# Performance work log

Hardware: AMD Instinct MI355X
Metric: run time of the kernel (lower is better)

## Reference

```python
import jax, jax.numpy as jnp
import numpy as np
import math

BT, N, D, H = 16, 1024, 128, 8
HD = D // H


def setup_inputs() -> dict:
    key = jax.random.key(0)
    ks = jax.random.split(key, 12)
    s = 1.0 / math.sqrt(D)
    return {
        "x": jax.random.normal(ks[0], (BT, N, D), dtype=jnp.float32),
        "adj": jax.random.uniform(ks[1], (BT, N, N), dtype=jnp.float32),
        "Wq": jax.random.normal(ks[2], (D, D), dtype=jnp.float32) * s,
        "bq": jax.random.normal(ks[3], (D,), dtype=jnp.float32) * 0.01,
        "Wk": jax.random.normal(ks[4], (D, D), dtype=jnp.float32) * s,
        "bk": jax.random.normal(ks[5], (D,), dtype=jnp.float32) * 0.01,
        "Wv": jax.random.normal(ks[6], (D, D), dtype=jnp.float32) * s,
        "bv": jax.random.normal(ks[7], (D,), dtype=jnp.float32) * 0.01,
        "Wo": jax.random.normal(ks[8], (D, D), dtype=jnp.float32) * s,
        "bo": jax.random.normal(ks[9], (D,), dtype=jnp.float32) * 0.01,
    }


def reference(x, adj, Wq, bq, Wk, bk, Wv, bv, Wo, bo):
    bt, n, d = x.shape
    # projections (torch Linear: x @ W.T + b), split into heads -> (BT,H,N,HD)
    q = (x @ Wq.T + bq).reshape(bt, n, H, HD).transpose(0, 2, 1, 3)
    k = (x @ Wk.T + bk).reshape(bt, n, H, HD).transpose(0, 2, 1, 3)
    v = (x @ Wv.T + bv).reshape(bt, n, H, HD).transpose(0, 2, 1, 3)
    scores = jnp.einsum('bhnd,bhmd->bhnm', q, k) / math.sqrt(HD)  # (BT,H,N,N)
    mask = (adj == 0)[:, None, :, :]  # (BT,1,N,N)
    scores = jnp.where(mask, -jnp.inf, scores)
    attn = jax.nn.softmax(scores, axis=-1)
    attn = attn * adj[:, None, :, :]  # reweight by continuous causal strength
    attn = attn / (attn.sum(axis=-1, keepdims=True) + 1e-8)  # renormalize
    ctx = jnp.einsum('bhnm,bhmd->bhnd', attn, v)  # (BT,H,N,HD)
    ctx = ctx.transpose(0, 2, 1, 3).reshape(bt, n, d)
    return ctx @ Wo.T + bo
```

## Files before the change

kernel.cpp:

```cpp
#include <hip/hip_runtime.h>
#include <hip/hip_bf16.h>

#define BTC 16
#define NC 1024
#define DC 128
#define HC 8
#define HDC 16

typedef __attribute__((ext_vector_type(8)))  short bf16x8;
typedef __attribute__((ext_vector_type(4)))  float f32x4;
typedef __attribute__((ext_vector_type(16))) float f32x16;
typedef __attribute__((ext_vector_type(4)))  short short4v;

#if __has_builtin(__builtin_amdgcn_exp2f)
#define EXP2F(x) __builtin_amdgcn_exp2f(x)
#else
#define EXP2F(x) exp2f(x)
#endif

#define QSCALE 0.36067376022224085f

union PK2 { short4v s4; __hip_bfloat162 h2[2]; };
union PK8 { bf16x8 v; short s[8]; __hip_bfloat162 h2[4]; };

static __device__ inline short f2bf(float f) {
    unsigned u = __builtin_bit_cast(unsigned, f);
    u += 0x7fffu + ((u >> 16) & 1u);
    return (short)(u >> 16);
}

static __device__ inline bf16x8 pack8f(float4 a, float4 b) {
    PK8 f;
    f.h2[0] = __float22bfloat162_rn(make_float2(a.x, a.y));
    f.h2[1] = __float22bfloat162_rn(make_float2(a.z, a.w));
    f.h2[2] = __float22bfloat162_rn(make_float2(b.x, b.y));
    f.h2[3] = __float22bfloat162_rn(make_float2(b.z, b.w));
    return f.v;
}

__global__ __launch_bounds__(256)
void proj_qkv(const float* __restrict__ x,
              const float* __restrict__ Wq, const float* __restrict__ bq,
              const float* __restrict__ Wk, const float* __restrict__ bk,
              const float* __restrict__ Wv, const float* __restrict__ bv,
              short* __restrict__ qo, short* __restrict__ ko, short* __restrict__ vto)
{
    const int y = blockIdx.y;
    const float* W    = (y == 0) ? Wq : (y == 1) ? Wk : Wv;
    const float* bias = (y == 0) ? bq : (y == 1) ? bk : bv;
    const float scale = (y == 0) ? QSCALE : 1.0f;

    const int tid  = threadIdx.x;
    const int wave = tid >> 6;
    const int lane = tid & 63;
    const int l15  = lane & 15;
    const int quad = lane >> 4;
    const int rowA = blockIdx.x * 64 + wave * 16;

    f32x4 acc[8];
#pragma unroll
    for (int t = 0; t < 8; ++t) acc[t] = (f32x4){0.f, 0.f, 0.f, 0.f};

#pragma unroll
    for (int kk = 0; kk < DC; kk += 32) {
        const float* xp = &x[(size_t)(rowA + l15) * DC + kk + quad * 8];
        bf16x8 Af = pack8f(*(const float4*)xp, *(const float4*)(xp + 4));
#pragma unroll
        for (int t = 0; t < 8; ++t) {
            const float* wp = &W[(size_t)(t * 16 + l15) * DC + kk + quad * 8];
            bf16x8 Bf = pack8f(*(const float4*)wp, *(const float4*)(wp + 4));
            acc[t] = __builtin_amdgcn_mfma_f32_16x16x32_bf16(Af, Bf, acc[t], 0, 0, 0);
        }
    }

#pragma unroll
    for (int t = 0; t < 8; ++t) {
        int c = t * 16 + l15;
        float b = bias[c];
#pragma unroll
        for (int r = 0; r < 4; ++r) {
            int row = rowA + quad * 4 + r;
            float val = (acc[t][r] + b) * scale;
            if (y == 2)
                vto[(size_t)(row >> 10) * (DC * NC) + (size_t)c * NC + (row & (NC - 1))] = f2bf(val);
            else
                ((y == 0) ? qo : ko)[(size_t)row * DC + c] = f2bf(val);
        }
    }
}

__global__ __launch_bounds__(512, 4)
void attn_fused(const short* __restrict__ qb, const short* __restrict__ kb,
                const short* __restrict__ vt, const float* __restrict__ adj,
                const float* __restrict__ Wo, const float* __restrict__ bo,
                float* __restrict__ out)
{
    __shared__ float As[2][32 * 132];
    __shared__ short Ps[8][32 * 40];
    __shared__ short Cs[32 * 136];

    const int tid  = threadIdx.x;
    const int wave = tid >> 6;
    const int lane = tid & 63;
    const int l15  = lane & 15;
    const int quad = lane >> 4;
    const int l31  = lane & 31;
    const int lh   = lane >> 5;
    const int bt   = blockIdx.y;
    const int qt0  = blockIdx.x * 32;
    const int h    = wave;

    const size_t xb = (size_t)bt * NC * DC;
    const size_t ab = (size_t)bt * NC * NC;

    bf16x8 Bq = *(const bf16x8*)&qb[xb + (size_t)(qt0 + l31) * DC + h * HDC + lh * 8];

    PK8 ones;
#pragma unroll
    for (int j = 0; j < 8; ++j) ones.s[j] = (short)0x3F80;

    f32x4 Cc[2], Cw[2];
#pragma unroll
    for (int s = 0; s < 2; ++s) {
        Cc[s] = (f32x4){0.f, 0.f, 0.f, 0.f};
        Cw[s] = (f32x4){0.f, 0.f, 0.f, 0.f};
    }

    const int arow = tid >> 4;
    const int acol = (tid & 15) * 8;
    const float* aptr = adj + ab + (size_t)(qt0 + arow) * NC + acol;
    float4 a0 = *(const float4*)aptr;
    float4 a1 = *(const float4*)(aptr + 4);

    short* Pw = &Ps[wave][0];
    const f32x16 z16 = {0.f,0.f,0.f,0.f,0.f,0.f,0.f,0.f,0.f,0.f,0.f,0.f,0.f,0.f,0.f,0.f};

    for (int ss = 0; ss < 8; ++ss) {
        const int p = ss & 1;
        *(float4*)&As[p][arow * 132 + acol]     = a0;
        *(float4*)&As[p][arow * 132 + acol + 4] = a1;
        __syncthreads();
        if (ss < 7) {
            a0 = *(const float4*)(aptr + (ss + 1) * 128);
            a1 = *(const float4*)(aptr + (ss + 1) * 128 + 4);
        }

        const int jt0 = ss * 128;
        bf16x8 Kf[4], Vf[4];
#pragma unroll
        for (int jj = 0; jj < 4; ++jj) {
            Kf[jj] = *(const bf16x8*)&kb[xb + (size_t)(jt0 + jj * 32 + l31) * DC + h * HDC + lh * 8];
            Vf[jj] = *(const bf16x8*)&vt[((size_t)bt * DC + h * HDC + l15) * NC + jt0 + jj * 32 + quad * 8];
        }

#pragma unroll
        for (int jj = 0; jj < 4; ++jj) {
            f32x16 S = __builtin_amdgcn_mfma_f32_32x32x16_bf16(Kf[jj], Bq, z16, 0, 0, 0);

#pragma unroll
            for (int rr = 0; rr < 4; ++rr) {
                int keyb = 8 * rr + 4 * lh;
                float4 a4 = *(const float4*)&As[p][l31 * 132 + jj * 32 + keyb];
                float p0 = EXP2F(S[4 * rr + 0]) * a4.x;
                float p1 = EXP2F(S[4 * rr + 1]) * a4.y;
                float p2 = EXP2F(S[4 * rr + 2]) * a4.z;
                float p3 = EXP2F(S[4 * rr + 3]) * a4.w;
                PK2 pk;
                pk.h2[0] = __float22bfloat162_rn(make_float2(p0, p1));
                pk.h2[1] = __float22bfloat162_rn(make_float2(p2, p3));
                *(short4v*)&Pw[l31 * 40 + keyb] = pk.s4;
            }
            __builtin_amdgcn_wave_barrier();

#pragma unroll
            for (int s = 0; s < 2; ++s) {
                bf16x8 Ap = *(const bf16x8*)&Pw[(s * 16 + l15) * 40 + quad * 8];
                Cc[s] = __builtin_amdgcn_mfma_f32_16x16x32_bf16(Ap, Vf[jj], Cc[s], 0, 0, 0);
                Cw[s] = __builtin_amdgcn_mfma_f32_16x16x32_bf16(Ap, ones.v, Cw[s], 0, 0, 0);
            }
            __builtin_amdgcn_wave_barrier();
        }
    }

#pragma unroll
    for (int s = 0; s < 2; ++s)
#pragma unroll
        for (int r = 0; r < 4; ++r) {
            float den = Cw[s][r];
            float rcp = den > 0.f ? 1.f / den : 0.f;
            int row = s * 16 + quad * 4 + r;
            Cs[row * 136 + h * HDC + l15] = f2bf(Cc[s][r] * rcp);
        }
    __syncthreads();

    const int rows0 = (wave & 1) * 16;
    const int tbase = wave >> 1;
    f32x4 oacc[2];
    oacc[0] = (f32x4){0.f, 0.f, 0.f, 0.f};
    oacc[1] = (f32x4){0.f, 0.f, 0.f, 0.f};

#pragma unroll
    for (int kk = 0; kk < DC; kk += 32) {
        bf16x8 Ac = *(const bf16x8*)&Cs[(rows0 + l15) * 136 + kk + quad * 8];
#pragma unroll
        for (int ti = 0; ti < 2; ++ti) {
            int t = tbase + ti * 4;
            const float* wp = &Wo[(size_t)(t * 16 + l15) * DC + kk + quad * 8];
            bf16x8 Bf = pack8f(*(const float4*)wp, *(const float4*)(wp + 4));
            oacc[ti] = __builtin_amdgcn_mfma_f32_16x16x32_bf16(Ac, Bf, oacc[ti], 0, 0, 0);
        }
    }

#pragma unroll
    for (int ti = 0; ti < 2; ++ti) {
        int c = (tbase + ti * 4) * 16 + l15;
        float b = bo[c];
#pragma unroll
        for (int r = 0; r < 4; ++r) {
            int row = qt0 + rows0 + quad * 4 + r;
            out[((size_t)bt * NC + row) * DC + c] = oacc[ti][r] + b;
        }
    }
}

extern "C" void kernel_launch(void* const* d_in, const int* in_sizes, int n_in,
                              void* d_out, int out_size, void* d_ws, size_t ws_size,
                              hipStream_t stream)
{
    const float* x   = (const float*)d_in[0];
    const float* adj = (const float*)d_in[1];
    const float* Wq  = (const float*)d_in[2];
    const float* bq  = (const float*)d_in[3];
    const float* Wk  = (const float*)d_in[4];
    const float* bk  = (const float*)d_in[5];
    const float* Wv  = (const float*)d_in[6];
    const float* bv  = (const float*)d_in[7];
    const float* Wo  = (const float*)d_in[8];
    const float* bo  = (const float*)d_in[9];
    float* out = (float*)d_out;

    const size_t tok = (size_t)BTC * NC * DC;
    short* qbuf = (short*)d_ws;
    short* kbuf = qbuf + tok;
    short* vt   = kbuf + tok;

    dim3 pgrid(256, 3);
    proj_qkv<<<pgrid, 256, 0, stream>>>(x, Wq, bq, Wk, bk, Wv, bv, qbuf, kbuf, vt);

    dim3 agrid(NC / 32, BTC);
    attn_fused<<<agrid, 512, 0, stream>>>(qbuf, kbuf, vt, adj, Wo, bo, out);
}
```

Measured before the change: 186.9 us.

## Split key range across two wave groups, read adj directly, sum weights in registers

The attention kernel now runs 1024 threads, with two groups of 8 waves each covering half of the key range for every head. The partial numerators and denominators are then combined through shared memory. The adjacency tile is read straight from global memory into registers instead of being staged in double-buffered LDS with block-wide barriers. The MFMA against a ones vector that computed the row sums is replaced by scalar register accumulation plus a shuffle. The P tile in LDS is XOR-swizzled to avoid bank conflicts. These changes add parallelism and remove a barrier per key tile, at the cost of an extra reduction step, a larger block, and uncoalesced-looking direct adj loads.

```diff
diff --git a/kernel.cpp b/kernel.cpp
--- a/kernel.cpp
+++ b/kernel.cpp
@@ -89,136 +89,127 @@
     }
 }
 
-__global__ __launch_bounds__(512, 4)
+__global__ __launch_bounds__(1024, 8)
 void attn_fused(const short* __restrict__ qb, const short* __restrict__ kb,
                 const short* __restrict__ vt, const float* __restrict__ adj,
                 const float* __restrict__ Wo, const float* __restrict__ bo,
                 float* __restrict__ out)
 {
-    __shared__ float As[2][32 * 132];
-    __shared__ short Ps[8][32 * 40];
+    __shared__ short Ps[16][32 * 40];
+    __shared__ float Rs[HC][32][17];
+    __shared__ float Ws[2][HC][32];
     __shared__ short Cs[32 * 136];
 
-    const int tid  = threadIdx.x;
-    const int wave = tid >> 6;
-    const int lane = tid & 63;
-    const int l15  = lane & 15;
-    const int quad = lane >> 4;
-    const int l31  = lane & 31;
-    const int lh   = lane >> 5;
-    const int bt   = blockIdx.y;
-    const int qt0  = blockIdx.x * 32;
-    const int h    = wave;
+    const int tid   = threadIdx.x;
+    const int wave  = tid >> 6;
+    const int lane  = tid & 63;
+    const int l15   = lane & 15;
+    const int quad  = lane >> 4;
+    const int l31   = lane & 31;
+    const int lh    = lane >> 5;
+    const int h     = wave & 7;
+    const int khalf = wave >> 3;
+    const int bt    = blockIdx.y;
+    const int qt0   = blockIdx.x * 32;
 
     const size_t xb = (size_t)bt * NC * DC;
     const size_t ab = (size_t)bt * NC * NC;
 
     bf16x8 Bq = *(const bf16x8*)&qb[xb + (size_t)(qt0 + l31) * DC + h * HDC + lh * 8];
 
-    PK8 ones;
-#pragma unroll
-    for (int j = 0; j < 8; ++j) ones.s[j] = (short)0x3F80;
-
-    f32x4 Cc[2], Cw[2];
-#pragma unroll
-    for (int s = 0; s < 2; ++s) {
-        Cc[s] = (f32x4){0.f, 0.f, 0.f, 0.f};
-        Cw[s] = (f32x4){0.f, 0.f, 0.f, 0.f};
-    }
-
-    const int arow = tid >> 4;
-    const int acol = (tid & 15) * 8;
-    const float* aptr = adj + ab + (size_t)(qt0 + arow) * NC + acol;
-    float4 a0 = *(const float4*)aptr;
-    float4 a1 = *(const float4*)(aptr + 4);
+    f32x4 Cc[2];
+    Cc[0] = (f32x4){0.f, 0.f, 0.f, 0.f};
+    Cc[1] = (f32x4){0.f, 0.f, 0.f, 0.f};
+    float wacc = 0.f;
 
     short* Pw = &Ps[wave][0];
-    const f32x16 z16 = {0.f,0.f,0.f,0.f,0.f,0.f,0.f,0.f,0.f,0.f,0.f,0.f,0.f,0.f,0.f,0.f};
-
-    for (int ss = 0; ss < 8; ++ss) {
-        const int p = ss & 1;
-        *(float4*)&As[p][arow * 132 + acol]     = a0;
-        *(float4*)&As[p][arow * 132 + acol + 4] = a1;
-        __syncthreads();
-        if (ss < 7) {
-            a0 = *(const float4*)(aptr + (ss + 1) * 128);
-            a1 = *(const float4*)(aptr + (ss + 1) * 128 + 4);
-        }
-
-        const int jt0 = ss * 128;
-        bf16x8 Kf[4], Vf[4];
-#pragma unroll
-        for (int jj = 0; jj < 4; ++jj) {
-            Kf[jj] = *(const bf16x8*)&kb[xb + (size_t)(jt0 + jj * 32 + l31) * DC + h * HDC + lh * 8];
-            Vf[jj] = *(const bf16x8*)&vt[((size_t)bt * DC + h * HDC + l15) * NC + jt0 + jj * 32 + quad * 8];
-        }
-
-#pragma unroll
-        for (int jj = 0; jj < 4; ++jj) {
-            f32x16 S = __builtin_amdgcn_mfma_f32_32x32x16_bf16(Kf[jj], Bq, z16, 0, 0, 0);
-
-#pragma unroll
-            for (int rr = 0; rr < 4; ++rr) {
-                int keyb = 8 * rr + 4 * lh;
-                float4 a4 = *(const float4*)&As[p][l31 * 132 + jj * 32 + keyb];
-                float p0 = EXP2F(S[4 * rr + 0]) * a4.x;
-                float p1 = EXP2F(S[4 * rr + 1]) * a4.y;
-                float p2 = EXP2F(S[4 * rr + 2]) * a4.z;
-                float p3 = EXP2F(S[4 * rr + 3]) * a4.w;
-                PK2 pk;
-                pk.h2[0] = __float22bfloat162_rn(make_float2(p0, p1));
-                pk.h2[1] = __float22bfloat162_rn(make_float2(p2, p3));
-                *(short4v*)&Pw[l31 * 40 + keyb] = pk.s4;
+    const int sw_w = (l31 >> 3) & 3;
+    const f32x16 z16 = {0.f,0.f,0.f,0.f,0.f,0.f,0.f,0.f,
+                        0.f,0.f,0.f,0.f,0.f,0.f,0.f,0.f};
+
+    const short* kbase = &kb[xb + h * HDC + lh * 8];
+    const short* vbase = &vt[((size_t)bt * DC + h * HDC + l15) * NC];
+    const float* abase = &adj[ab + (size_t)(qt0 + l31) * NC + 4 * lh];
+
+    for (int jj = 0; jj < 16; ++jj) {
+        const int jt = khalf * 512 + jj * 32;
+
+        bf16x8 Kf = *(const bf16x8*)&kbase[(size_t)(jt + l31) * DC];
+        bf16x8 Vf = *(const bf16x8*)&vbase[jt + quad * 8];
+        float4 a4[4];
+#pragma unroll
+        for (int rr = 0; rr < 4; ++rr)
+            a4[rr] = *(const float4*)&abase[jt + 8 * rr];
+
+        f32x16 S = __builtin_amdgcn_mfma_f32_32x32x16_bf16(Kf, Bq, z16, 0, 0, 0);
+
+#pragma unroll
+        for (int rr = 0; rr < 4; ++rr) {
+            float p0 = EXP2F(S[4 * rr + 0]) * a4[rr].x;
+            float p1 = EXP2F(S[4 * rr + 1]) * a4[rr].y;
+            float p2 = EXP2F(S[4 * rr + 2]) * a4[rr].z;
+            float p3 = EXP2F(S[4 * rr + 3]) * a4[rr].w;
+            wacc += (p0 + p1) + (p2 + p3);
+            PK2 pk;
+            pk.h2[0] = __float22bfloat162_rn(make_float2(p0, p1));
+            pk.h2[1] = __float22bfloat162_rn(make_float2(p2, p3));
+            *(short4v*)&Pw[l31 * 40 + (rr ^ sw_w) * 8 + lh * 4] = pk.s4;
+        }
+        __builtin_amdgcn_wave_barrier();
+
+#pragma unroll
+        for (int s = 0; s < 2; ++s) {
+            int R = s * 16 + l15;
+            bf16x8 Ap = *(const bf16x8*)&Pw[R * 40 + (quad ^ ((R >> 3) & 3)) * 8];
+            Cc[s] = __builtin_amdgcn_mfma_f32_16x16x32_bf16(Ap, Vf, Cc[s], 0, 0, 0);
+        }
+        __builtin_amdgcn_wave_barrier();
+    }
+
+    wacc += __shfl_xor(wacc, 32, 64);
+    if (lane < 32) Ws[khalf][h][l31] = wacc;
+    if (khalf == 1) {
+#pragma unroll
+        for (int s = 0; s < 2; ++s)
+#pragma unroll
+            for (int r = 0; r < 4; ++r)
+                Rs[h][s * 16 + quad * 4 + r][l15] = Cc[s][r];
+    }
+    __syncthreads();
+
+    if (khalf == 0) {
+#pragma unroll
+        for (int s = 0; s < 2; ++s)
+#pragma unroll
+            for (int r = 0; r < 4; ++r) {
+                int row = s * 16 + quad * 4 + r;
+                float num = Cc[s][r] + Rs[h][row][l15];
+                float den = Ws[0][h][row] + Ws[1][h][row];
+                float rcp = den > 0.f ? 1.f / den : 0.f;
+                Cs[row * 136 + h * HDC + l15] = f2bf(num * rcp);
             }
-            __builtin_amdgcn_wave_barrier();
-
-#pragma unroll
-            for (int s = 0; s < 2; ++s) {
-                bf16x8 Ap = *(const bf16x8*)&Pw[(s * 16 + l15) * 40 + quad * 8];
-                Cc[s] = __builtin_amdgcn_mfma_f32_16x16x32_bf16(Ap, Vf[jj], Cc[s], 0, 0, 0);
-                Cw[s] = __builtin_amdgcn_mfma_f32_16x16x32_bf16(Ap, ones.v, Cw[s], 0, 0, 0);
-            }
-            __builtin_amdgcn_wave_barrier();
-        }
-    }
-
-#pragma unroll
-    for (int s = 0; s < 2; ++s)
-#pragma unroll
-        for (int r = 0; r < 4; ++r) {
-            float den = Cw[s][r];
-            float rcp = den > 0.f ? 1.f / den : 0.f;
-            int row = s * 16 + quad * 4 + r;
-            Cs[row * 136 + h * HDC + l15] = f2bf(Cc[s][r] * rcp);
-        }
+    }
     __syncthreads();
 
     const int rows0 = (wave & 1) * 16;
-    const int tbase = wave >> 1;
-    f32x4 oacc[2];
-    oacc[0] = (f32x4){0.f, 0.f, 0.f, 0.f};
-    oacc[1] = (f32x4){0.f, 0.f, 0.f, 0.f};
+    const int t     = wave >> 1;
+    f32x4 oacc = (f32x4){0.f, 0.f, 0.f, 0.f};
 
 #pragma unroll
     for (int kk = 0; kk < DC; kk += 32) {
         bf16x8 Ac = *(const bf16x8*)&Cs[(rows0 + l15) * 136 + kk + quad * 8];
-#pragma unroll
-        for (int ti = 0; ti < 2; ++ti) {
-            int t = tbase + ti * 4;
-            const float* wp = &Wo[(size_t)(t * 16 + l15) * DC + kk + quad * 8];
-            bf16x8 Bf = pack8f(*(const float4*)wp, *(const float4*)(wp + 4));
-            oacc[ti] = __builtin_amdgcn_mfma_f32_16x16x32_bf16(Ac, Bf, oacc[ti], 0, 0, 0);
-        }
-    }
-
-#pragma unroll
-    for (int ti = 0; ti < 2; ++ti) {
-        int c = (tbase + ti * 4) * 16 + l15;
+        const float* wp = &Wo[(size_t)(t * 16 + l15) * DC + kk + quad * 8];
+        bf16x8 Bf = pack8f(*(const float4*)wp, *(const float4*)(wp + 4));
+        oacc = __builtin_amdgcn_mfma_f32_16x16x32_bf16(Ac, Bf, oacc, 0, 0, 0);
+    }
+
+    {
+        int c = t * 16 + l15;
         float b = bo[c];
 #pragma unroll
         for (int r = 0; r < 4; ++r) {
             int row = qt0 + rows0 + quad * 4 + r;
-            out[((size_t)bt * NC + row) * DC + c] = oacc[ti][r] + b;
+            out[((size_t)bt * NC + row) * DC + c] = oacc[r] + b;
         }
     }
 }
@@ -248,5 +239,5 @@
     proj_qkv<<<pgrid, 256, 0, stream>>>(x, Wq, bq, Wk, bk, Wv, bv, qbuf, kbuf, vt);
 
     dim3 agrid(NC / 32, BTC);
-    attn_fused<<<agrid, 512, 0, stream>>>(qbuf, kbuf, vt, adj, Wo, bo, out);
-}
+    attn_fused<<<agrid, 1024, 0, stream>>>(qbuf, kbuf, vt, adj, Wo, bo, out);
+}
```

After: 289.8 us. 1.55x slower.
